# Kernel optimization log

Hardware: AMD Instinct MI355X
Metric: run time of the kernel (lower is better)

## Reference

```python
import jax, jax.numpy as jnp
import numpy as np

EPS = 1e-5  # BatchNorm1d eps


def _glorot(key, shape):
    fan_in, fan_out = shape[0], shape[1]
    lim = float(np.sqrt(6.0 / (fan_in + fan_out)))
    return jax.random.uniform(key, shape, jnp.float32, -lim, lim)


def setup_inputs() -> dict:
    key = jax.random.key(0)
    ks = jax.random.split(key, 6)
    N, IN, H, OUT = 50000, 128, 64, 64
    E = 800000
    x = jax.random.normal(ks[0], (N, IN), jnp.float32)
    edge_index = jax.random.randint(ks[1], (2, E), 0, N, jnp.int64)
    return {
        "x": x,
        "edge_index": edge_index,
        "W1": _glorot(ks[2], (IN, H)),
        "b1": jnp.zeros((H,), jnp.float32),
        "gamma1": jnp.ones((H,), jnp.float32),
        "beta1": jnp.zeros((H,), jnp.float32),
        "W2": _glorot(ks[3], (H, OUT)),
        "b2": jnp.zeros((OUT,), jnp.float32),
        "gamma2": jnp.ones((OUT,), jnp.float32),
        "beta2": jnp.zeros((OUT,), jnp.float32),
    }


def _gcn_conv(x, W, b, src, dst, norm, n):
    # x' = D^{-1/2} (A + I) D^{-1/2} X W + b  (PyG GCNConv, edge_weight=None)
    h = x @ W                              # [N, F]
    msg = h[src] * norm[:, None]           # gather + scale, [E+N, F]
    out = jax.ops.segment_sum(msg, dst, num_segments=n)  # scatter-add
    return out + b


def _batch_norm(h, gamma, beta):
    # training-mode BN over node dim, biased variance (as torch uses for normalization)
    mean = h.mean(0)
    var = h.var(0)
    return (h - mean) * jax.lax.rsqrt(var + EPS) * gamma + beta


def reference(x, edge_index, W1, b1, gamma1, beta1, W2, b2, gamma2, beta2):
    n = x.shape[0]
    # add self loops
    loop = jnp.arange(n, dtype=edge_index.dtype)
    src = jnp.concatenate([edge_index[0], loop])
    dst = jnp.concatenate([edge_index[1], loop])
    # symmetric degree normalization (deg >= 1 thanks to self loops)
    deg = jax.ops.segment_sum(jnp.ones(src.shape[0], x.dtype), dst, num_segments=n)
    dinv = jax.lax.rsqrt(jnp.maximum(deg, 1e-12))
    norm = dinv[src] * dinv[dst]           # [E+N]

    # layer 1: GCNConv -> BN -> ReLU (dropout = identity in eval)
    h = _gcn_conv(x, W1, b1, src, dst, norm, n)
    h = jax.nn.relu(_batch_norm(h, gamma1, beta1))
    # layer 2: GCNConv -> BN (no activation on last layer)
    h = _gcn_conv(h, W2, b2, src, dst, norm, n)
    h = _batch_norm(h, gamma2, beta2)
    return h
```

## Files before the change

### kernel.cpp

```cpp
#include <hip/hip_runtime.h>
#include <hip/hip_fp16.h>
#include <math.h>

#define EPS 1e-5f
#define CAP 64

typedef float v4f __attribute__((ext_vector_type(4)));
typedef unsigned int u32x4 __attribute__((ext_vector_type(4)));
typedef _Float16 half8 __attribute__((ext_vector_type(8)));
typedef float f32x4 __attribute__((ext_vector_type(4)));

__device__ __forceinline__ float xor32sum(float a) {
    return a + __shfl_xor(a, 32, 64);
}

__global__ void k_init(int* __restrict__ cnt, float* __restrict__ stats,
                       __half* __restrict__ Ylo, __half* __restrict__ Yhi, int N) {
    int i = blockIdx.x * blockDim.x + threadIdx.x;
    if (i < N) cnt[i] = 0;
    if (i < 256) stats[i] = 0.0f;
    if (i < 16) {
        ((int*)(Ylo + (size_t)N * 32))[i] = 0;
        ((int*)(Yhi + (size_t)N * 32))[i] = 0;
    }
}

__global__ __launch_bounds__(256) void k_gemm1_fill(const float* __restrict__ x,
                                                    const float* __restrict__ W1,
                                                    __half* __restrict__ Ylo,
                                                    __half* __restrict__ Yhi, int N,
                                                    const int* __restrict__ src,
                                                    const int* __restrict__ dst,
                                                    int* __restrict__ cnt,
                                                    unsigned short* __restrict__ csr,
                                                    int E, int G) {
    if ((int)blockIdx.x >= G) {
        int t = (blockIdx.x - G) * 256 + threadIdx.x;
        int stride = (gridDim.x - G) * 256;
        for (int e = t; e < E; e += stride) {
            int d = dst[e];
            int pos = atomicAdd(&cnt[d], 1);
            if (pos < CAP)
                __builtin_nontemporal_store((unsigned short)src[e], &csr[(size_t)d * CAP + pos]);
        }
        return;
    }
    int lane = threadIdx.x & 63;
    int wave = threadIdx.x >> 6;
    int ln15 = lane & 15;
    int kg = lane >> 4;
    half8 Bf[4][4];
#pragma unroll
    for (int kt = 0; kt < 4; ++kt)
#pragma unroll
        for (int ct = 0; ct < 4; ++ct) {
            half8 b;
#pragma unroll
            for (int j = 0; j < 8; ++j)
                b[j] = (_Float16)W1[(size_t)(kt * 32 + kg * 8 + j) * 64 + ct * 16 + ln15];
            Bf[kt][ct] = b;
        }
    int nrb = (N + 15) >> 4;
    int gw = blockIdx.x * 4 + wave;
    int nwv = G * 4;
    for (int rb = gw; rb < nrb; rb += nwv) {
        int row = min(rb * 16 + ln15, N - 1);
        const float4* xr = (const float4*)(x + (size_t)row * 128);
        f32x4 acc[4];
#pragma unroll
        for (int ct = 0; ct < 4; ++ct) acc[ct] = (f32x4){0.f, 0.f, 0.f, 0.f};
#pragma unroll
        for (int kt = 0; kt < 4; ++kt) {
            float4 v0 = xr[kt * 8 + kg * 2];
            float4 v1 = xr[kt * 8 + kg * 2 + 1];
            half8 A;
            A[0] = (_Float16)v0.x; A[1] = (_Float16)v0.y;
            A[2] = (_Float16)v0.z; A[3] = (_Float16)v0.w;
            A[4] = (_Float16)v1.x; A[5] = (_Float16)v1.y;
            A[6] = (_Float16)v1.z; A[7] = (_Float16)v1.w;
#pragma unroll
            for (int ct = 0; ct < 4; ++ct)
                acc[ct] = __builtin_amdgcn_mfma_f32_16x16x32_f16(A, Bf[kt][ct], acc[ct], 0, 0, 0);
        }
#pragma unroll
        for (int ct = 0; ct < 4; ++ct) {
            int col = ct * 16 + ln15;
            __half* Yo = (col >= 32) ? Yhi : Ylo;
            int cc = col & 31;
#pragma unroll
            for (int i = 0; i < 4; ++i) {
                int gr = rb * 16 + kg * 4 + i;
                if (gr < N) Yo[(size_t)gr * 32 + cc] = __float2half(acc[ct][i]);
            }
        }
    }
}

__global__ void k_scale(const int* __restrict__ cnt, float* __restrict__ dinv,
                        __half* __restrict__ Ylo, __half* __restrict__ Yhi, int N) {
    int i = blockIdx.x * blockDim.x + threadIdx.x;
    if (i == 0) dinv[N] = 0.0f;
    int row = i >> 2, c4 = i & 3;
    if (row >= N) return;
    float dv = rsqrtf((float)(cnt[row] + 1));
    if (c4 == 0) dinv[row] = dv;
    union U16 { uint4 u; __half2 h[4]; } t;
#pragma unroll
    for (int buf = 0; buf < 2; ++buf) {
        __half* Y = buf ? Yhi : Ylo;
        uint4* p = (uint4*)(Y + (size_t)row * 32 + c4 * 8);
        t.u = *p;
#pragma unroll
        for (int k = 0; k < 4; ++k) {
            float2 f = __half22float2(t.h[k]);
            t.h[k] = __float22half2_rn(make_float2(f.x * dv, f.y * dv));
        }
        *p = t.u;
    }
}

template <bool HALF_OUT>
__global__ __launch_bounds__(256) void k_agg(const __half* __restrict__ Ylo,
                                             const __half* __restrict__ Yhi,
                                             const unsigned short* __restrict__ csr,
                                             const int* __restrict__ cnt,
                                             const float* __restrict__ dinv,
                                             void* __restrict__ Hout,
                                             float* __restrict__ stats, int N) {
    __shared__ float ssum[4][32], ssq[4][32];
    int half = blockIdx.x & 1;
    const __half* Y = half ? Yhi : Ylo;
    int lane = threadIdx.x & 63;
    int wave = threadIdx.x >> 6;
    int fl = lane & 3;
    int node = (lane >> 2) & 3;
    int g = lane >> 4;
    int gd = g >> 1;
    int gsh = (g & 1) << 4;
    float selfmask = (g == 0) ? 1.f : 0.f;
    int slot = (blockIdx.x >> 1) * 4 + wave;
    int nslots = (gridDim.x >> 1) * 4;
    float s[8], q[8];
#pragma unroll
    for (int j = 0; j < 8; ++j) { s[j] = 0.f; q[j] = 0.f; }
    union U16 { uint4 u; __half2 h[4]; };
    for (int base = slot * 4; base < N; base += nslots * 4) {
        int myv = base + node;
        bool vok = myv < N;
        int vs = vok ? myv : N;
        int c  = vok ? min(cnt[myv], CAP) : 0;
        float dv = dinv[vs];
        const unsigned int* crow =
            (const unsigned int*)(csr + (size_t)(vok ? myv : 0) * CAP);
        float a[8];
        {
            U16 t; t.u = *(const uint4*)(Y + (size_t)vs * 32 + fl * 8);
#pragma unroll
            for (int k = 0; k < 4; ++k) {
                float2 f = __half22float2(t.h[k]);
                a[2 * k]     = selfmask * f.x;
                a[2 * k + 1] = selfmask * f.y;
            }
        }
        for (int b = 0; b < 16; ++b) {
            if (__all(4 * b >= c)) break;
            unsigned int w = crow[2 * b + gd];
            bool live = vok && (4 * b + g < c);
            int ent = live ? (int)((w >> gsh) & 0xFFFFu) : 0xFFFF;
            int idx = min(ent, N);
            U16 t; t.u = *(const uint4*)(Y + (size_t)idx * 32 + fl * 8);
#pragma unroll
            for (int k = 0; k < 4; ++k) {
                float2 f = __half22float2(t.h[k]);
                a[2 * k]     += f.x;
                a[2 * k + 1] += f.y;
            }
        }
#pragma unroll
        for (int j = 0; j < 8; ++j) {
            a[j] += __shfl_xor(a[j], 16, 64);
            a[j] = xor32sum(a[j]) * dv;
        }
        if (g == 0 && vok) {
            if (HALF_OUT) {
                __half* H1 = (__half*)Hout;
                union { u32x4 u; __half2 h[4]; } o;
#pragma unroll
                for (int k = 0; k < 4; ++k)
                    o.h[k] = __floats2half2_rn(a[2 * k], a[2 * k + 1]);
                __builtin_nontemporal_store(o.u,
                    (u32x4*)(H1 + (size_t)myv * 64 + half * 32 + fl * 8));
            } else {
                float* H = (float*)Hout;
                v4f lo = {a[0], a[1], a[2], a[3]};
                v4f hi = {a[4], a[5], a[6], a[7]};
                float* dst = H + (size_t)myv * 64 + half * 32 + fl * 8;
                __builtin_nontemporal_store(lo, (v4f*)dst);
                __builtin_nontemporal_store(hi, (v4f*)(dst + 4));
            }
        }
#pragma unroll
        for (int j = 0; j < 8; ++j) { s[j] += a[j]; q[j] += a[j] * a[j]; }
    }
#pragma unroll
    for (int j = 0; j < 8; ++j) {
        s[j] += __shfl_xor(s[j], 4, 64); s[j] += __shfl_xor(s[j], 8, 64);
        q[j] += __shfl_xor(q[j], 4, 64); q[j] += __shfl_xor(q[j], 8, 64);
    }
    if (lane < 4) {
#pragma unroll
        for (int j = 0; j < 8; ++j) {
            ssum[wave][fl * 8 + j] = s[j];
            ssq[wave][fl * 8 + j]  = q[j];
        }
    }
    __syncthreads();
    if (threadIdx.x < 32) {
        float ts = ssum[0][threadIdx.x] + ssum[1][threadIdx.x] + ssum[2][threadIdx.x] + ssum[3][threadIdx.x];
        float tq = ssq[0][threadIdx.x] + ssq[1][threadIdx.x] + ssq[2][threadIdx.x] + ssq[3][threadIdx.x];
        atomicAdd(&stats[half * 32 + threadIdx.x], ts);
        atomicAdd(&stats[64 + half * 32 + threadIdx.x], tq);
    }
}

__global__ __launch_bounds__(256) void k_gemm2(const __half* __restrict__ H1,
                                               const float* __restrict__ stats,
                                               const float* __restrict__ gamma,
                                               const float* __restrict__ beta,
                                               const float* __restrict__ W2,
                                               const float* __restrict__ dinv,
                                               __half* __restrict__ Ylo,
                                               __half* __restrict__ Yhi, int N) {
    __shared__ float w[64 * 64];
    __shared__ float xs[4][64][4];
    for (int i = threadIdx.x; i < 64 * 64; i += 256) w[i] = W2[i];
    int lane = threadIdx.x & 63;
    int wave = threadIdx.x >> 6;
    int half = lane >> 5, l = lane & 31;
    __half* Yout = half ? Yhi : Ylo;
    float mean = stats[lane] / (float)N;
    float var = stats[64 + lane] / (float)N - mean * mean;
    float rstd = rsqrtf(var + EPS);
    float scale = rstd * gamma[lane];
    float shift = beta[lane] - mean * scale;
    __syncthreads();
    int gwave = blockIdx.x * 4 + wave;
    int nw = gridDim.x * 4;
    for (int r0 = gwave * 4; r0 < N; r0 += nw * 4) {
        int nr = min(4, N - r0);
#pragma unroll
        for (int j = 0; j < 4; ++j) {
            float v = 0.f;
            if (j < nr) {
                v = __half2float(H1[(size_t)(r0 + j) * 64 + lane]);
                v = fmaxf(v * scale + shift, 0.f);
            }
            xs[wave][lane][j] = v;
        }
        float a0 = 0.f, a1 = 0.f, a2 = 0.f, a3 = 0.f;
#pragma unroll 8
        for (int k = 0; k < 64; ++k) {
            float wk = w[k * 64 + lane];
            float4 xv = *(const float4*)&xs[wave][k][0];
            a0 += xv.x * wk; a1 += xv.y * wk; a2 += xv.z * wk; a3 += xv.w * wk;
        }
        Yout[(size_t)(r0 + 0) * 32 + l] = __float2half(a0 * dinv[r0]);
        if (nr > 1) Yout[(size_t)(r0 + 1) * 32 + l] = __float2half(a1 * dinv[r0 + 1]);
        if (nr > 2) Yout[(size_t)(r0 + 2) * 32 + l] = __float2half(a2 * dinv[r0 + 2]);
        if (nr > 3) Yout[(size_t)(r0 + 3) * 32 + l] = __float2half(a3 * dinv[r0 + 3]);
    }
}

__global__ void k_bnfinal(float* __restrict__ out, const float* __restrict__ stats,
                          const float* __restrict__ gamma, const float* __restrict__ beta,
                          int N) {
    int i = blockIdx.x * blockDim.x + threadIdx.x;
    int total = N * 64;
    if (i < total) {
        int f = i & 63;
        float mean = stats[f] / (float)N;
        float var = stats[64 + f] / (float)N - mean * mean;
        float rstd = rsqrtf(var + EPS);
        out[i] = (out[i] - mean) * rstd * gamma[f] + beta[f];
    }
}

extern "C" void kernel_launch(void* const* d_in, const int* in_sizes, int n_in,
                              void* d_out, int out_size, void* d_ws, size_t ws_size,
                              hipStream_t stream) {
    const float* x      = (const float*)d_in[0];
    const int*   ei     = (const int*)d_in[1];
    const float* W1     = (const float*)d_in[2];
    const float* gamma1 = (const float*)d_in[4];
    const float* beta1  = (const float*)d_in[5];
    const float* W2     = (const float*)d_in[6];
    const float* gamma2 = (const float*)d_in[8];
    const float* beta2  = (const float*)d_in[9];
    float* out = (float*)d_out;

    const int N = in_sizes[0] / 128;
    const int E = in_sizes[1] / 2;
    const int* src = ei;
    const int* dst = ei + E;

    char* ws = (char*)d_ws;
    int*   cnt   = (int*)  ws;
    float* stats = (float*)(ws + 0x40000);
    float* dinv  = (float*)(ws + 0x50000);
    __half* Ylo  = (__half*)(ws + 0x90000);
    __half* Yhi  = (__half*)(ws + 0x90000 + 0x320000);
    __half* H1   = (__half*)(ws + 0x90000 + 0x640000);
    unsigned short* csr = (unsigned short*)(ws + 0x90000 + 0x640000 + 0xC40000);

    const int B = (N + 255) / 256;
    const int total = N * 64;
    const int G = 768, F = 256;

    k_init<<<B, 256, 0, stream>>>(cnt, stats, Ylo, Yhi, N);

    k_gemm1_fill<<<G + F, 256, 0, stream>>>(x, W1, Ylo, Yhi, N, src, dst, cnt, csr, E, G);
    k_scale<<<(N * 4 + 255) / 256, 256, 0, stream>>>(cnt, dinv, Ylo, Yhi, N);
    k_agg<true><<<1250, 256, 0, stream>>>(Ylo, Yhi, csr, cnt, dinv, H1, stats, N);

    k_gemm2<<<1024, 256, 0, stream>>>(H1, stats, gamma1, beta1, W2, dinv, Ylo, Yhi, N);
    k_agg<false><<<1250, 256, 0, stream>>>(Ylo, Yhi, csr, cnt, dinv, out, stats + 128, N);
    k_bnfinal<<<(total + 255) / 256, 256, 0, stream>>>(out, stats + 128, gamma2, beta2, N);
}
```

Measured before the change: 254.4 us.

## Use MFMA f16 for second-layer GEMM and unroll CSR fill loop

Rewrites k_gemm2 to use 16x16x32 f16 MFMA with W2 fragments held in registers, fusing the BN+ReLU of layer 1 into the A-fragment load and dropping shared-memory staging. The grid is resized to 784 blocks to match 16-row tiles. The edge-fill loop is also unrolled by four so that loads and atomics from independent edges can overlap. This adds f16 rounding of the normalized activations before the matmul, and the dinv float4 read can run past N on the last tile.

```diff
diff --git a/kernel.cpp b/kernel.cpp
--- a/kernel.cpp
+++ b/kernel.cpp
@@ -37,7 +37,20 @@
     if ((int)blockIdx.x >= G) {
         int t = (blockIdx.x - G) * 256 + threadIdx.x;
         int stride = (gridDim.x - G) * 256;
-        for (int e = t; e < E; e += stride) {
+        int e = t;
+        for (; e + 3 * stride < E; e += 4 * stride) {
+            int d0 = dst[e], d1 = dst[e + stride], d2 = dst[e + 2 * stride], d3 = dst[e + 3 * stride];
+            int s0 = src[e], s1 = src[e + stride], s2 = src[e + 2 * stride], s3 = src[e + 3 * stride];
+            int p0 = atomicAdd(&cnt[d0], 1);
+            int p1 = atomicAdd(&cnt[d1], 1);
+            int p2 = atomicAdd(&cnt[d2], 1);
+            int p3 = atomicAdd(&cnt[d3], 1);
+            if (p0 < CAP) __builtin_nontemporal_store((unsigned short)s0, &csr[(size_t)d0 * CAP + p0]);
+            if (p1 < CAP) __builtin_nontemporal_store((unsigned short)s1, &csr[(size_t)d1 * CAP + p1]);
+            if (p2 < CAP) __builtin_nontemporal_store((unsigned short)s2, &csr[(size_t)d2 * CAP + p2]);
+            if (p3 < CAP) __builtin_nontemporal_store((unsigned short)s3, &csr[(size_t)d3 * CAP + p3]);
+        }
+        for (; e < E; e += stride) {
             int d = dst[e];
             int pos = atomicAdd(&cnt[d], 1);
             if (pos < CAP)
@@ -231,43 +244,70 @@
                                                const float* __restrict__ dinv,
                                                __half* __restrict__ Ylo,
                                                __half* __restrict__ Yhi, int N) {
-    __shared__ float w[64 * 64];
-    __shared__ float xs[4][64][4];
-    for (int i = threadIdx.x; i < 64 * 64; i += 256) w[i] = W2[i];
     int lane = threadIdx.x & 63;
     int wave = threadIdx.x >> 6;
-    int half = lane >> 5, l = lane & 31;
-    __half* Yout = half ? Yhi : Ylo;
-    float mean = stats[lane] / (float)N;
-    float var = stats[64 + lane] / (float)N - mean * mean;
-    float rstd = rsqrtf(var + EPS);
-    float scale = rstd * gamma[lane];
-    float shift = beta[lane] - mean * scale;
-    __syncthreads();
-    int gwave = blockIdx.x * 4 + wave;
-    int nw = gridDim.x * 4;
-    for (int r0 = gwave * 4; r0 < N; r0 += nw * 4) {
-        int nr = min(4, N - r0);
-#pragma unroll
-        for (int j = 0; j < 4; ++j) {
-            float v = 0.f;
-            if (j < nr) {
-                v = __half2float(H1[(size_t)(r0 + j) * 64 + lane]);
-                v = fmaxf(v * scale + shift, 0.f);
-            }
-            xs[wave][lane][j] = v;
-        }
-        float a0 = 0.f, a1 = 0.f, a2 = 0.f, a3 = 0.f;
-#pragma unroll 8
-        for (int k = 0; k < 64; ++k) {
-            float wk = w[k * 64 + lane];
-            float4 xv = *(const float4*)&xs[wave][k][0];
-            a0 += xv.x * wk; a1 += xv.y * wk; a2 += xv.z * wk; a3 += xv.w * wk;
-        }
-        Yout[(size_t)(r0 + 0) * 32 + l] = __float2half(a0 * dinv[r0]);
-        if (nr > 1) Yout[(size_t)(r0 + 1) * 32 + l] = __float2half(a1 * dinv[r0 + 1]);
-        if (nr > 2) Yout[(size_t)(r0 + 2) * 32 + l] = __float2half(a2 * dinv[r0 + 2]);
-        if (nr > 3) Yout[(size_t)(r0 + 3) * 32 + l] = __float2half(a3 * dinv[r0 + 3]);
+    int ln15 = lane & 15;
+    int kg = lane >> 4;
+    float sc[2][8], sh[2][8];
+#pragma unroll
+    for (int kt = 0; kt < 2; ++kt)
+#pragma unroll
+        for (int j = 0; j < 8; ++j) {
+            int k = kt * 32 + kg * 8 + j;
+            float mean = stats[k] / (float)N;
+            float var = stats[64 + k] / (float)N - mean * mean;
+            float s = rsqrtf(var + EPS) * gamma[k];
+            sc[kt][j] = s;
+            sh[kt][j] = beta[k] - mean * s;
+        }
+    half8 Bf[2][4];
+#pragma unroll
+    for (int kt = 0; kt < 2; ++kt)
+#pragma unroll
+        for (int ct = 0; ct < 4; ++ct) {
+            half8 b;
+#pragma unroll
+            for (int j = 0; j < 8; ++j)
+                b[j] = (_Float16)W2[(size_t)(kt * 32 + kg * 8 + j) * 64 + ct * 16 + ln15];
+            Bf[kt][ct] = b;
+        }
+    int nrb = (N + 15) >> 4;
+    int gw = blockIdx.x * 4 + wave;
+    int nwv = gridDim.x * 4;
+    for (int rb = gw; rb < nrb; rb += nwv) {
+        int row = min(rb * 16 + ln15, N - 1);
+        const __half* hr = H1 + (size_t)row * 64;
+        f32x4 acc[4];
+#pragma unroll
+        for (int ct = 0; ct < 4; ++ct) acc[ct] = (f32x4){0.f, 0.f, 0.f, 0.f};
+#pragma unroll
+        for (int kt = 0; kt < 2; ++kt) {
+            union { uint4 u; __half h[8]; } t;
+            t.u = *(const uint4*)(hr + kt * 32 + kg * 8);
+            half8 A;
+#pragma unroll
+            for (int j = 0; j < 8; ++j) {
+                float v = __half2float(t.h[j]);
+                v = fmaxf(v * sc[kt][j] + sh[kt][j], 0.f);
+                A[j] = (_Float16)v;
+            }
+#pragma unroll
+            for (int ct = 0; ct < 4; ++ct)
+                acc[ct] = __builtin_amdgcn_mfma_f32_16x16x32_f16(A, Bf[kt][ct], acc[ct], 0, 0, 0);
+        }
+        float4 dv4 = *(const float4*)(dinv + rb * 16 + kg * 4);
+#pragma unroll
+        for (int ct = 0; ct < 4; ++ct) {
+            int col = ct * 16 + ln15;
+            __half* Yo = (col >= 32) ? Yhi : Ylo;
+            int cc = col & 31;
+#pragma unroll
+            for (int i = 0; i < 4; ++i) {
+                int gr = rb * 16 + kg * 4 + i;
+                float dvv = (i == 0) ? dv4.x : (i == 1) ? dv4.y : (i == 2) ? dv4.z : dv4.w;
+                if (gr < N) Yo[(size_t)gr * 32 + cc] = __float2half(acc[ct][i] * dvv);
+            }
+        }
     }
 }
 
@@ -322,7 +362,7 @@
     k_scale<<<(N * 4 + 255) / 256, 256, 0, stream>>>(cnt, dinv, Ylo, Yhi, N);
     k_agg<true><<<1250, 256, 0, stream>>>(Ylo, Yhi, csr, cnt, dinv, H1, stats, N);
 
-    k_gemm2<<<1024, 256, 0, stream>>>(H1, stats, gamma1, beta1, W2, dinv, Ylo, Yhi, N);
+    k_gemm2<<<784, 256, 0, stream>>>(H1, stats, gamma1, beta1, W2, dinv, Ylo, Yhi, N);
     k_agg<false><<<1250, 256, 0, stream>>>(Ylo, Yhi, csr, cnt, dinv, out, stats + 128, N);
     k_bnfinal<<<(total + 255) / 256, 256, 0, stream>>>(out, stats + 128, gamma2, beta2, N);
 }
```

Result: slower. 265.2 us (+4.2%).
